# Kernel optimization log

Hardware: AMD Instinct MI355X
Metric: run time of the kernel (lower is better)

Reference implementation:

```python
import jax, jax.numpy as jnp
import numpy as np

B, K, W, H = 32, 64, 100, 150
ALPHA = 0.2        # leaky-relu slope
THRES = 2e-4       # causal threshold


def setup_inputs() -> dict:
    ks = jax.random.split(jax.random.key(0), 20)
    s = 0.1
    inp = {
        "x": jax.random.normal(ks[0], (B, K, W), jnp.float32),
        "y": jax.random.normal(ks[1], (B, K, 1), jnp.float32),
        "z_noise": jax.random.normal(ks[2], (B, H), jnp.float32),
        "lin_w": jax.random.normal(ks[3], (W, W), jnp.float32) * s,
        "lin_b": jax.random.normal(ks[4], (W,), jnp.float32) * s,
        "a": jax.random.normal(ks[5], (2, 1), jnp.float32),
        "bias": jax.random.normal(ks[6], (K, K * W), jnp.float32) * 0.01,
        "gl_wih": jax.random.normal(ks[7], (3 * H, W), jnp.float32) * s,
        "gl_whh": jax.random.normal(ks[8], (3 * H, H), jnp.float32) * s,
        "gl_bih": jax.random.normal(ks[9], (3 * H,), jnp.float32) * s,
        "gl_bhh": jax.random.normal(ks[10], (3 * H,), jnp.float32) * s,
        "mu_w": jax.random.normal(ks[11], (H, H), jnp.float32) * s,
        "mu_b": jax.random.normal(ks[12], (H,), jnp.float32) * s,
        "std_w": jax.random.normal(ks[13], (H, H), jnp.float32) * s,
        "std_b": jax.random.normal(ks[14], (H,), jnp.float32) * s,
        "net_wih": jax.random.normal(ks[15], (K, 3 * H, W), jnp.float32) * s,
        "net_whh": jax.random.normal(ks[16], (K, 3 * H, H), jnp.float32) * s,
        "net_bih": jax.random.normal(ks[17], (K, 3 * H), jnp.float32) * s,
        "net_bhh": jax.random.normal(ks[18], (K, 3 * H), jnp.float32) * s,
    }
    return inp


def _gru_last(wih, whh, bih, bhh, xs, h0):
    # xs: [B, S, in], h0: [B, H] -> final hidden [B, H]. PyTorch gate order r,z,n.
    gx = jnp.einsum('bsi,gi->sbg', xs, wih) + bih  # [S, B, 3H]
    h_dim = h0.shape[-1]

    def step(h, g):
        gh = h @ whh.T + bhh
        r = jax.nn.sigmoid(g[:, :h_dim] + gh[:, :h_dim])
        z = jax.nn.sigmoid(g[:, h_dim:2 * h_dim] + gh[:, h_dim:2 * h_dim])
        n = jnp.tanh(g[:, 2 * h_dim:] + r * gh[:, 2 * h_dim:])
        return (1.0 - z) * n + z * h, None

    h_last, _ = jax.lax.scan(step, h0, gx)
    return h_last


def reference(x, y, z_noise, lin_w, lin_b, a, bias, gl_wih, gl_whh, gl_bih, gl_bhh,
              mu_w, mu_b, std_w, std_b, net_wih, net_whh, net_bih, net_bhh):
    xw = x[:, :, -W:]
    Wx = xw @ lin_w.T + lin_b                       # [B, K, W]
    v = Wx.reshape(Wx.shape[0], K * W)              # [B, K*W]
    # e = a_input @ a, where a_input[...,0]=y broadcast, a_input[...,1]=v tiled per node
    e = a[0, 0] * y + a[1, 0] * v[:, None, :] + bias  # [B, K, K*W]
    e = jax.nn.leaky_relu(e, ALPHA)
    attention = jax.nn.softmax(e, axis=2)           # dropout p=0 -> identity
    A = attention >= THRES                           # [B, K, K*W] mask
    Ax = jnp.where(A, v[:, None, :], 0.0)
    cause_x = Wx + Ax.sum(axis=2, keepdims=True)    # [B, K, W]
    # left GRU over the node dimension (seq len = K)
    h0 = jnp.zeros((cause_x.shape[0], H), cause_x.dtype)
    h_t = _gru_last(gl_wih, gl_whh, gl_bih, gl_bhh, cause_x, h0)  # [B, H]
    mu = h_t @ mu_w.T + mu_b
    log_var = h_t @ std_w.T + std_b
    sigma = jnp.exp(0.5 * log_var)
    z = mu + sigma * z_noise                        # [B, H]
    # K independent GRUs, same input Wx and same init state z -> vmap over weights
    causes = jax.vmap(lambda wi, wh, bi, bh: _gru_last(wi, wh, bi, bh, Wx, z))(
        net_wih, net_whh, net_bih, net_bhh)         # [K, B, H]
    return causes.transpose(1, 0, 2)                # [B, K, H]
```

## Files before the change

kernel.cpp:

```cpp
#include <hip/hip_runtime.h>

#define Bc 32
#define Kc 64
#define Wc 100
#define Hc 150
#define H3c 450
#define KWc 6400
#define ALPHAc 0.2f
#define THRESc 0.0002f

typedef unsigned int u32;
typedef unsigned short u16;
typedef __attribute__((ext_vector_type(8))) short short8;
typedef __attribute__((ext_vector_type(4))) float floatx4;

#define OFF_WX      0u
#define OFF_CS      204800u
#define OFF_GX      206848u
#define OFF_HT      1128448u
#define OFF_Z       1133248u

__device__ __forceinline__ float us2f(u16 u){ u32 x=((u32)u)<<16; return __uint_as_float(x); }
__device__ __forceinline__ u16 f2us(float f){
  u32 x = __float_as_uint(f);
  u32 r = (x + 0x7fffu + ((x>>16)&1u)) >> 16;
  return (u16)r;
}

__device__ __forceinline__ void lds_barrier(){
  __builtin_amdgcn_sched_barrier(0);
  asm volatile("s_waitcnt lgkmcnt(0)" ::: "memory");
  __builtin_amdgcn_s_barrier();
  __builtin_amdgcn_sched_barrier(0);
}

__global__ void wx_kernel(const float* __restrict__ x, const float* __restrict__ lin_w,
                          const float* __restrict__ lin_b, float* __restrict__ ws){
  int o = blockIdx.x*256 + threadIdx.x;
  if (o >= Bc*KWc) return;
  int i = o % Wc;
  int bk = o / Wc;
  const float4* xr = (const float4*)(x + bk*Wc);
  const float4* wr = (const float4*)(lin_w + i*Wc);
  float acc = lin_b[i];
  #pragma unroll
  for (int j=0;j<25;j++){
    float4 xv = xr[j], wv = wr[j];
    acc += xv.x*wv.x + xv.y*wv.y + xv.z*wv.z + xv.w*wv.w;
  }
  ws[OFF_WX + o] = acc;
}

__global__ void attn_kernel(const float* __restrict__ y, const float* __restrict__ a,
                            const float* __restrict__ bias, float* __restrict__ ws){
  __shared__ __align__(16) float e_l[KWc];
  __shared__ float red[4];
  int row = blockIdx.x;
  int b = row >> 6, k = row & 63;
  int tid = threadIdx.x;
  float a0 = a[0], a1 = a[1];
  float yv = y[row];
  const float4* v4  = (const float4*)(ws + OFF_WX + (size_t)b*KWc);
  const float4* br4 = (const float4*)(bias + (size_t)k*KWc);
  float4* e4 = (float4*)e_l;
  float ay = a0*yv;
  float m = -3.4e38f;
  for (int j=tid; j<KWc/4; j+=256){
    float4 vv = v4[j], bb = br4[j];
    float4 e;
    e.x = ay + a1*vv.x + bb.x; e.x = (e.x>=0.f)?e.x:ALPHAc*e.x;
    e.y = ay + a1*vv.y + bb.y; e.y = (e.y>=0.f)?e.y:ALPHAc*e.y;
    e.z = ay + a1*vv.z + bb.z; e.z = (e.z>=0.f)?e.z:ALPHAc*e.z;
    e.w = ay + a1*vv.w + bb.w; e.w = (e.w>=0.f)?e.w:ALPHAc*e.w;
    e4[j] = e;
    m = fmaxf(m, fmaxf(fmaxf(e.x,e.y), fmaxf(e.z,e.w)));
  }
  for (int o=32;o;o>>=1) m = fmaxf(m, __shfl_down(m, o));
  if ((tid&63)==0) red[tid>>6] = m;
  __syncthreads();
  m = fmaxf(fmaxf(red[0],red[1]), fmaxf(red[2],red[3]));
  __syncthreads();
  float ssum = 0.f;
  for (int j=tid; j<KWc/4; j+=256){
    float4 e = e4[j];
    ssum += __expf(e.x-m) + __expf(e.y-m) + __expf(e.z-m) + __expf(e.w-m);
  }
  for (int o=32;o;o>>=1) ssum += __shfl_down(ssum, o);
  if ((tid&63)==0) red[tid>>6] = ssum;
  __syncthreads();
  float s = red[0]+red[1]+red[2]+red[3];
  float thr = m + logf(THRESc * s);
  float cs = 0.f;
  for (int j=tid; j<KWc/4; j+=256){
    float4 e = e4[j];
    float4 vv = v4[j];
    if (e.x >= thr) cs += vv.x;
    if (e.y >= thr) cs += vv.y;
    if (e.z >= thr) cs += vv.z;
    if (e.w >= thr) cs += vv.w;
  }
  for (int o=32;o;o>>=1) cs += __shfl_down(cs, o);
  if ((tid&63)==0) red[tid>>6] = cs;
  __syncthreads();
  if (tid==0) ws[OFF_CS + row] = red[0]+red[1]+red[2]+red[3];
}

__global__ void glproj_kernel(const float* __restrict__ gl_wih, const float* __restrict__ gl_bih,
                              float* __restrict__ ws){
  int o = blockIdx.x*256 + threadIdx.x;
  if (o >= Kc*Bc*H3c) return;
  int g = o % H3c;
  int t = o / H3c;
  int b = t & 31, s = t >> 5;
  float cs = ws[OFF_CS + b*Kc + s];
  const float4* xr = (const float4*)(ws + OFF_WX + b*KWc + s*Wc);
  const float4* wr = (const float4*)(gl_wih + g*Wc);
  float acc = gl_bih[g];
  #pragma unroll
  for (int j=0;j<25;j++){
    float4 wv = wr[j], xv = xr[j];
    acc += (xv.x+cs)*wv.x + (xv.y+cs)*wv.y + (xv.z+cs)*wv.z + (xv.w+cs)*wv.w;
  }
  ws[OFF_GX + o] = acc;
}

__global__ void __launch_bounds__(1024,1) glgru4_kernel(
    const float* __restrict__ gl_whh, const float* __restrict__ gl_bhh,
    float* __restrict__ ws){
  __shared__ __align__(16) u16 bF[10*16*40];
  __shared__ float g_l[480*10];
  int b0 = blockIdx.x*8;
  int tid = threadIdx.x;
  int w = tid >> 6, lane = tid & 63, quad = lane >> 4, n16 = lane & 15;

  short8 whhA[2][5];
  #pragma unroll
  for (int ti=0; ti<2; ti++){
    int tile = w*2 + ti;
    int sec = tile/10;
    int sr = (tile - sec*10)*16 + n16;
    bool rowok = (tile < 30) && (sr < Hc);
    int grow = (sec<3 ? sec : 2)*Hc + sr;
    const float* wr = gl_whh + (size_t)grow*Hc;
    #pragma unroll
    for (int c=0;c<5;c++){
      union { short8 v; u16 u[8]; } t8;
      #pragma unroll
      for (int j2=0;j2<4;j2++){
        int kk2 = c*32 + quad*8 + j2*2;
        float2 wv = (rowok && (kk2+1) < Hc) ? *(const float2*)(wr + kk2) : make_float2(0.f,0.f);
        t8.u[j2*2]   = f2us(wv.x);
        t8.u[j2*2+1] = f2us(wv.y);
      }
      whhA[ti][c] = t8.v;
    }
  }
  for (int i=tid; i<10*16*40/2; i+=1024) ((u32*)bF)[i] = 0u;

  float hst[2] = {0.f,0.f};
  float bh_r[2], bh_z[2], bh_n[2];
  int tT[2], tBL[2];
  #pragma unroll
  for (int q=0;q<2;q++){
    int task = tid + q*1024;
    if (task < 1200){
      int bl = task/150, t = task - bl*150;
      tT[q] = t; tBL[q] = bl;
      bh_r[q] = gl_bhh[t];
      bh_z[q] = gl_bhh[Hc+t];
      bh_n[q] = gl_bhh[2*Hc+t];
    } else { tT[q] = 0; tBL[q] = -1; }
  }

  for (int s=0;s<Kc;s++){
    lds_barrier();
    float gxr[2], gxz[2], gxn[2];
    const float* gxb = ws + OFF_GX + (size_t)(s*Bc)*H3c;
    #pragma unroll
    for (int q=0;q<2;q++){
      if (tBL[q] >= 0){
        const float* gp = gxb + (size_t)(b0+tBL[q])*H3c;
        int t = tT[q];
        gxr[q] = gp[t]; gxz[q] = gp[Hc+t]; gxn[q] = gp[2*Hc+t];
      }
    }
    const u16* bBase = bF + (size_t)n16*40 + (size_t)quad*8;
    short8 bh[10];
    #pragma unroll
    for (int c=0;c<10;c++) bh[c] = *(const short8*)(bBase + (size_t)c*640);
    floatx4 acc[2] = {{0.f,0.f,0.f,0.f},{0.f,0.f,0.f,0.f}};
    #pragma unroll
    for (int c=0;c<10;c++){
      int ca = (c<5)? c : (c-5);
      #pragma unroll
      for (int ti=0;ti<2;ti++)
        acc[ti] = __builtin_amdgcn_mfma_f32_16x16x32_bf16(whhA[ti][ca], bh[c], acc[ti], 0,0,0);
    }
    if (n16 < 8){
      #pragma unroll
      for (int ti=0;ti<2;ti++){
        int tile = w*2 + ti;
        if (tile < 30){
          int row0 = tile*16 + quad*4;
          float* gp = g_l + row0*10 + n16;
          #pragma unroll
          for (int r=0;r<4;r++) gp[r*10] = acc[ti][r];
        }
      }
    }
    lds_barrier();
    #pragma unroll
    for (int q=0;q<2;q++){
      if (tBL[q] >= 0){
        int t = tT[q], bl = tBL[q];
        float a_r = gxr[q] + g_l[t*10+bl] + bh_r[q];
        float a_z = gxz[q] + g_l[(160+t)*10+bl] + bh_z[q];
        float r  = 1.f/(1.f+__expf(-a_r));
        float zz = 1.f/(1.f+__expf(-a_z));
        float nx = gxn[q] + r*(g_l[(320+t)*10+bl] + bh_n[q]);
        nx = fminf(fmaxf(nx,-15.f),15.f);
        float e2 = __expf(2.f*nx);
        float n = (e2-1.f)/(e2+1.f);
        float h = (1.f-zz)*n + zz*hst[q];
        hst[q] = h;
        u16 hi = f2us(h); float hif = us2f(hi); u16 lo = f2us(h - hif);
        bF[(t>>5)*640 + bl*40 + (t&31)] = hi;
        bF[(5+(t>>5))*640 + bl*40 + (t&31)] = lo;
      }
    }
  }
  #pragma unroll
  for (int q=0;q<2;q++){
    if (tBL[q] >= 0)
      ws[OFF_HT + (size_t)(b0+tBL[q])*Hc + tT[q]] = hst[q];
  }
}

__global__ void z_kernel(const float* __restrict__ z_noise, const float* __restrict__ mu_w,
                         const float* __restrict__ mu_b, const float* __restrict__ std_w,
                         const float* __restrict__ std_b, float* __restrict__ ws){
  int o = blockIdx.x*256 + threadIdx.x;
  if (o >= Bc*Hc) return;
  int t = o % Hc, b = o / Hc;
  const float* h = ws + OFF_HT + b*Hc;
  const float2* mwr = (const float2*)(mu_w + t*Hc);
  const float2* swr = (const float2*)(std_w + t*Hc);
  float mu = mu_b[t], lv = std_b[t];
  for (int j=0;j<Hc/2;j++){
    float2 mw = mwr[j], sw = swr[j];
    float h0 = h[2*j], h1 = h[2*j+1];
    mu += h0*mw.x + h1*mw.y;
    lv += h0*sw.x + h1*sw.y;
  }
  float sg = expf(0.5f*lv);
  ws[OFF_Z + o] = mu + sg*z_noise[o];
}

__global__ void __launch_bounds__(1024,1) causes3_kernel(
    const float* __restrict__ net_wih, const float* __restrict__ net_whh,
    const float* __restrict__ net_bih, const float* __restrict__ net_bhh,
    const float* __restrict__ ws, float* __restrict__ out){
  __shared__ __align__(16) u16 bF[14*16*40];
  __shared__ float g_rz[320*10];
  __shared__ float g_nh[160*10];
  __shared__ float g_np[160*10];
  int kk = blockIdx.x & 63, bg = blockIdx.x >> 6, b0 = bg*8;
  int tid = threadIdx.x;
  int w = tid >> 6, lane = tid & 63, quad = lane >> 4, n16 = lane & 15;
  const float* whhk = net_whh + (size_t)kk*H3c*Hc;
  const float* wihk = net_wih + (size_t)kk*H3c*Wc;
  const float* bihk = net_bih + kk*H3c;
  const float* bhhk = net_bhh + kk*H3c;

  short8 whhA[2][5], wihA[2][4];
  #pragma unroll
  for (int ti=0; ti<2; ti++){
    int tile = w*2 + ti;
    int sec = tile/10;
    int sr = (tile - sec*10)*16 + n16;
    bool rowok = (tile < 30) && (sr < Hc);
    int grow = (sec<3 ? sec : 2)*Hc + sr;
    #pragma unroll
    for (int c=0;c<5;c++){
      union { short8 v; u16 u[8]; } t8;
      #pragma unroll
      for (int j=0;j<8;j++){
        int k = c*32 + quad*8 + j;
        float v = (rowok && k < Hc) ? whhk[(size_t)grow*Hc + k] : 0.f;
        t8.u[j] = f2us(v);
      }
      whhA[ti][c] = t8.v;
    }
    #pragma unroll
    for (int c=0;c<4;c++){
      union { short8 v; u16 u[8]; } t8;
      #pragma unroll
      for (int j=0;j<8;j++){
        int k = c*32 + quad*8 + j;
        float v = (rowok && k < Wc) ? wihk[(size_t)grow*Wc + k] : 0.f;
        t8.u[j] = f2us(v);
      }
      wihA[ti][c] = t8.v;
    }
  }

  for (int i=tid; i<14*16*40/2; i+=1024) ((u32*)bF)[i] = 0u;

  float hst[2] = {0.f,0.f};
  float brz_r[2], brz_z[2], bnh_[2], bnp_[2];
  #pragma unroll
  for (int q=0;q<2;q++){
    int task = tid + q*1024;
    if (task < 1200){
      int t = task >> 3, bb = task & 7;
      float h = ws[OFF_Z + (b0+bb)*Hc + t];
      hst[q] = h;
      brz_r[q] = bhhk[t]      + bihk[t];
      brz_z[q] = bhhk[Hc+t]   + bihk[Hc+t];
      bnh_[q]  = bhhk[2*Hc+t];
      bnp_[q]  = bihk[2*Hc+t];
      u16 hi = f2us(h); float hif = us2f(hi); u16 lo = f2us(h - hif);
      bF[(t>>5)*640 + bb*40 + (t&31)] = hi;
      bF[(5+(t>>5))*640 + bb*40 + (t&31)] = lo;
    } else { tT_dummy: ; }
  }
  if (tid < 800){
    int bb = tid/100, i = tid - bb*100;
    float xv = ws[OFF_WX + (b0+bb)*KWc + i];
    bF[(10+(i>>5))*640 + bb*40 + (i&31)] = f2us(xv);
  }

  bool xok = (tid < 800);
  int bb0 = xok ? tid/100 : 0;
  int i0  = tid - bb0*100;

  const bool isN = (w >= 10);
  for (int s=0;s<Kc;s++){
    float xp0 = 0.f;
    if (xok && s < Kc-1)
      xp0 = ws[OFF_WX + (size_t)(b0+bb0)*KWc + (s+1)*Wc + i0];
    lds_barrier();
    const u16* bBase = bF + (size_t)n16*40 + (size_t)quad*8;
    short8 bx[4];
    #pragma unroll
    for (int c=0;c<4;c++) bx[c] = *(const short8*)(bBase + (size_t)(10+c)*640);
    floatx4 acc[2] = {{0.f,0.f,0.f,0.f},{0.f,0.f,0.f,0.f}};
    #pragma unroll
    for (int ca=0;ca<4;ca++){
      #pragma unroll
      for (int ti=0;ti<2;ti++)
        acc[ti] = __builtin_amdgcn_mfma_f32_16x16x32_bf16(wihA[ti][ca], bx[ca], acc[ti], 0,0,0);
    }
    __builtin_amdgcn_sched_barrier(0);
    short8 bh0[5];
    #pragma unroll
    for (int c=0;c<5;c++) bh0[c] = *(const short8*)(bBase + (size_t)c*640);
    if (isN){
      if (n16 < 8){
        #pragma unroll
        for (int ti=0;ti<2;ti++){
          int tile = w*2 + ti;
          if (tile < 30){
            int srb = (tile - 20)*16 + quad*4;
            float* gq = g_np + srb*10 + n16;
            #pragma unroll
            for (int r=0;r<4;r++) gq[r*10] = acc[ti][r];
          }
        }
      }
      #pragma unroll
      for (int ti=0;ti<2;ti++) acc[ti] = (floatx4){0.f,0.f,0.f,0.f};
    }
    #pragma unroll
    for (int c=0;c<5;c++){
      #pragma unroll
      for (int ti=0;ti<2;ti++)
        acc[ti] = __builtin_amdgcn_mfma_f32_16x16x32_bf16(whhA[ti][c], bh0[c], acc[ti], 0,0,0);
    }
    __builtin_amdgcn_sched_barrier(0);
    short8 bh1[5];
    #pragma unroll
    for (int c=0;c<5;c++) bh1[c] = *(const short8*)(bBase + (size_t)(5+c)*640);
    #pragma unroll
    for (int c=0;c<5;c++){
      #pragma unroll
      for (int ti=0;ti<2;ti++)
        acc[ti] = __builtin_amdgcn_mfma_f32_16x16x32_bf16(whhA[ti][c], bh1[c], acc[ti], 0,0,0);
    }
    if (n16 < 8){
      #pragma unroll
      for (int ti=0;ti<2;ti++){
        int tile = w*2 + ti;
        if (tile < 30){
          int sec = tile/10;
          int srb = (tile - sec*10)*16 + quad*4;
          if (sec < 2){
            float* gp = g_rz + (sec*160 + srb)*10 + n16;
            #pragma unroll
            for (int r=0;r<4;r++) gp[r*10] = acc[ti][r];
          } else {
            float* gh = g_nh + srb*10 + n16;
            #pragma unroll
            for (int r=0;r<4;r++) gh[r*10] = acc[ti][r];
          }
        }
      }
    }
    lds_barrier();
    #pragma unroll
    for (int q=0;q<2;q++){
      int task = tid + q*1024;
      if (task < 1200){
        int t = task >> 3, bb = task & 7;
        float a_r = g_rz[t*10+bb] + brz_r[q];
        float a_z = g_rz[(160+t)*10+bb] + brz_z[q];
        float r  = 1.f/(1.f+__expf(-a_r));
        float zz = 1.f/(1.f+__expf(-a_z));
        float nx = (g_np[t*10+bb] + bnp_[q]) + r*(g_nh[t*10+bb] + bnh_[q]);
        nx = fminf(fmaxf(nx,-15.f),15.f);
        float e2 = __expf(2.f*nx);
        float n = (e2-1.f)/(e2+1.f);
        float h = (1.f-zz)*n + zz*hst[q];
        hst[q] = h;
        u16 hi = f2us(h); float hif = us2f(hi); u16 lo = f2us(h - hif);
        bF[(t>>5)*640 + bb*40 + (t&31)] = hi;
        bF[(5+(t>>5))*640 + bb*40 + (t&31)] = lo;
      }
    }
    if (xok && s < Kc-1)
      bF[(10+(i0>>5))*640 + bb0*40 + (i0&31)] = f2us(xp0);
  }
  #pragma unroll
  for (int q=0;q<2;q++){
    int task = tid + q*1024;
    if (task < 1200){
      int t = task >> 3, bb = task & 7;
      out[((size_t)(b0+bb)*Kc + kk)*Hc + t] = hst[q];
    }
  }
}

extern "C" void kernel_launch(void* const* d_in, const int* in_sizes, int n_in,
                              void* d_out, int out_size, void* d_ws, size_t ws_size,
                              hipStream_t stream){
  const float* x        = (const float*)d_in[0];
  const float* y        = (const float*)d_in[1];
  const float* z_noise  = (const float*)d_in[2];
  const float* lin_w    = (const float*)d_in[3];
  const float* lin_b    = (const float*)d_in[4];
  const float* a        = (const float*)d_in[5];
  const float* bias     = (const float*)d_in[6];
  const float* gl_wih   = (const float*)d_in[7];
  const float* gl_whh   = (const float*)d_in[8];
  const float* gl_bih   = (const float*)d_in[9];
  const float* gl_bhh   = (const float*)d_in[10];
  const float* mu_w     = (const float*)d_in[11];
  const float* mu_b     = (const float*)d_in[12];
  const float* std_w    = (const float*)d_in[13];
  const float* std_b    = (const float*)d_in[14];
  const float* net_wih  = (const float*)d_in[15];
  const float* net_whh  = (const float*)d_in[16];
  const float* net_bih  = (const float*)d_in[17];
  const float* net_bhh  = (const float*)d_in[18];
  float* ws = (float*)d_ws;
  float* out = (float*)d_out;

  wx_kernel<<<(Bc*KWc+255)/256, 256, 0, stream>>>(x, lin_w, lin_b, ws);
  attn_kernel<<<Bc*Kc, 256, 0, stream>>>(y, a, bias, ws);
  glproj_kernel<<<(Kc*Bc*H3c+255)/256, 256, 0, stream>>>(gl_wih, gl_bih, ws);
  glgru4_kernel<<<4, 1024, 0, stream>>>(gl_whh, gl_bhh, ws);
  z_kernel<<<(Bc*Hc+255)/256, 256, 0, stream>>>(z_noise, mu_w, mu_b, std_w, std_b, ws);
  causes3_kernel<<<Kc*4, 1024, 0, stream>>>(net_wih, net_whh, net_bih, net_bhh, ws, out);
}
```

Before: 487.8 us.

## Give each wave all three gates per hidden range; double-buffer state to drop barrier

```diff
diff --git a/kernel.cpp b/kernel.cpp
--- a/kernel.cpp
+++ b/kernel.cpp
@@ -11,6 +11,7 @@
 
 typedef unsigned int u32;
 typedef unsigned short u16;
+typedef unsigned long long u64;
 typedef __attribute__((ext_vector_type(8))) short short8;
 typedef __attribute__((ext_vector_type(4))) float floatx4;
 
@@ -124,115 +125,110 @@
   ws[OFF_GX + o] = acc;
 }
 
-__global__ void __launch_bounds__(1024,1) glgru4_kernel(
+__global__ void __launch_bounds__(640,1) glgru4_kernel(
     const float* __restrict__ gl_whh, const float* __restrict__ gl_bhh,
     float* __restrict__ ws){
-  __shared__ __align__(16) u16 bF[10*16*40];
-  __shared__ float g_l[480*10];
+  __shared__ __align__(16) u16 bF[20*16*40];
   int b0 = blockIdx.x*8;
   int tid = threadIdx.x;
   int w = tid >> 6, lane = tid & 63, quad = lane >> 4, n16 = lane & 15;
-
-  short8 whhA[2][5];
-  #pragma unroll
-  for (int ti=0; ti<2; ti++){
-    int tile = w*2 + ti;
-    int sec = tile/10;
-    int sr = (tile - sec*10)*16 + n16;
-    bool rowok = (tile < 30) && (sr < Hc);
-    int grow = (sec<3 ? sec : 2)*Hc + sr;
-    const float* wr = gl_whh + (size_t)grow*Hc;
+  int range = w;
+  int t0 = range*16 + quad*4;
+
+  short8 whhA[3][5];
+  #pragma unroll
+  for (int sec=0; sec<3; sec++){
+    int sr = range*16 + n16;
+    bool rowok = (sr < Hc);
+    const float* wr = gl_whh + (size_t)(sec*Hc + sr)*Hc;
     #pragma unroll
     for (int c=0;c<5;c++){
       union { short8 v; u16 u[8]; } t8;
       #pragma unroll
-      for (int j2=0;j2<4;j2++){
-        int kk2 = c*32 + quad*8 + j2*2;
-        float2 wv = (rowok && (kk2+1) < Hc) ? *(const float2*)(wr + kk2) : make_float2(0.f,0.f);
-        t8.u[j2*2]   = f2us(wv.x);
-        t8.u[j2*2+1] = f2us(wv.y);
-      }
-      whhA[ti][c] = t8.v;
-    }
-  }
-  for (int i=tid; i<10*16*40/2; i+=1024) ((u32*)bF)[i] = 0u;
-
-  float hst[2] = {0.f,0.f};
-  float bh_r[2], bh_z[2], bh_n[2];
-  int tT[2], tBL[2];
-  #pragma unroll
-  for (int q=0;q<2;q++){
-    int task = tid + q*1024;
-    if (task < 1200){
-      int bl = task/150, t = task - bl*150;
-      tT[q] = t; tBL[q] = bl;
-      bh_r[q] = gl_bhh[t];
-      bh_z[q] = gl_bhh[Hc+t];
-      bh_n[q] = gl_bhh[2*Hc+t];
-    } else { tT[q] = 0; tBL[q] = -1; }
+      for (int j=0;j<8;j++){
+        int k = c*32 + quad*8 + j;
+        float v = (rowok && k < Hc) ? wr[k] : 0.f;
+        t8.u[j] = f2us(v);
+      }
+      whhA[sec][c] = t8.v;
+    }
+  }
+  for (int i=tid; i<20*640/2; i+=640) ((u32*)bF)[i] = 0u;
+
+  float bh_r[4], bh_z[4], bh_n[4], hprev[4];
+  #pragma unroll
+  for (int r=0;r<4;r++){
+    int t = t0 + r;
+    bool ok = (t < Hc);
+    bh_r[r] = ok ? gl_bhh[t]      : 0.f;
+    bh_z[r] = ok ? gl_bhh[Hc+t]   : 0.f;
+    bh_n[r] = ok ? gl_bhh[2*Hc+t] : 0.f;
+    hprev[r] = 0.f;
   }
 
   for (int s=0;s<Kc;s++){
+    int rb = s & 1, wb = rb ^ 1;
+    float gxr[4], gxz[4], gxn[4];
+    if (n16 < 8){
+      const float* gp = ws + OFF_GX + (size_t)(s*Bc + b0 + n16)*H3c;
+      #pragma unroll
+      for (int r=0;r<4;r++){
+        int t = t0 + r;
+        bool ok = (t < Hc);
+        gxr[r] = ok ? gp[t]      : 0.f;
+        gxz[r] = ok ? gp[Hc+t]   : 0.f;
+        gxn[r] = ok ? gp[2*Hc+t] : 0.f;
+      }
+    }
     lds_barrier();
-    float gxr[2], gxz[2], gxn[2];
-    const float* gxb = ws + OFF_GX + (size_t)(s*Bc)*H3c;
-    #pragma unroll
-    for (int q=0;q<2;q++){
-      if (tBL[q] >= 0){
-        const float* gp = gxb + (size_t)(b0+tBL[q])*H3c;
-        int t = tT[q];
-        gxr[q] = gp[t]; gxz[q] = gp[Hc+t]; gxn[q] = gp[2*Hc+t];
-      }
-    }
-    const u16* bBase = bF + (size_t)n16*40 + (size_t)quad*8;
-    short8 bh[10];
-    #pragma unroll
-    for (int c=0;c<10;c++) bh[c] = *(const short8*)(bBase + (size_t)c*640);
-    floatx4 acc[2] = {{0.f,0.f,0.f,0.f},{0.f,0.f,0.f,0.f}};
-    #pragma unroll
-    for (int c=0;c<10;c++){
-      int ca = (c<5)? c : (c-5);
-      #pragma unroll
-      for (int ti=0;ti<2;ti++)
-        acc[ti] = __builtin_amdgcn_mfma_f32_16x16x32_bf16(whhA[ti][ca], bh[c], acc[ti], 0,0,0);
+    const u16* hBase = bF + (size_t)rb*6400 + (size_t)(n16&7)*40 + (size_t)(n16>>3)*3200 + (size_t)quad*8;
+    short8 bh[5];
+    #pragma unroll
+    for (int c=0;c<5;c++) bh[c] = *(const short8*)(hBase + (size_t)c*640);
+    floatx4 accR={0.f,0.f,0.f,0.f}, accZ={0.f,0.f,0.f,0.f}, accNH={0.f,0.f,0.f,0.f};
+    #pragma unroll
+    for (int c=0;c<5;c++){
+      accR  = __builtin_amdgcn_mfma_f32_16x16x32_bf16(whhA[0][c], bh[c], accR, 0,0,0);
+      accZ  = __builtin_amdgcn_mfma_f32_16x16x32_bf16(whhA[1][c], bh[c], accZ, 0,0,0);
+      accNH = __builtin_amdgcn_mfma_f32_16x16x32_bf16(whhA[2][c], bh[c], accNH, 0,0,0);
+    }
+    #pragma unroll
+    for (int r=0;r<4;r++){
+      accR[r]  += __shfl_xor(accR[r], 8);
+      accZ[r]  += __shfl_xor(accZ[r], 8);
+      accNH[r] += __shfl_xor(accNH[r], 8);
     }
     if (n16 < 8){
-      #pragma unroll
-      for (int ti=0;ti<2;ti++){
-        int tile = w*2 + ti;
-        if (tile < 30){
-          int row0 = tile*16 + quad*4;
-          float* gp = g_l + row0*10 + n16;
-          #pragma unroll
-          for (int r=0;r<4;r++) gp[r*10] = acc[ti][r];
-        }
-      }
-    }
-    lds_barrier();
-    #pragma unroll
-    for (int q=0;q<2;q++){
-      if (tBL[q] >= 0){
-        int t = tT[q], bl = tBL[q];
-        float a_r = gxr[q] + g_l[t*10+bl] + bh_r[q];
-        float a_z = gxz[q] + g_l[(160+t)*10+bl] + bh_z[q];
-        float r  = 1.f/(1.f+__expf(-a_r));
+      float hout[4];
+      #pragma unroll
+      for (int r=0;r<4;r++){
+        float a_r = gxr[r] + accR[r] + bh_r[r];
+        float a_z = gxz[r] + accZ[r] + bh_z[r];
+        float rr = 1.f/(1.f+__expf(-a_r));
         float zz = 1.f/(1.f+__expf(-a_z));
-        float nx = gxn[q] + r*(g_l[(320+t)*10+bl] + bh_n[q]);
+        float nx = gxn[r] + rr*(accNH[r] + bh_n[r]);
         nx = fminf(fmaxf(nx,-15.f),15.f);
         float e2 = __expf(2.f*nx);
         float n = (e2-1.f)/(e2+1.f);
-        float h = (1.f-zz)*n + zz*hst[q];
-        hst[q] = h;
-        u16 hi = f2us(h); float hif = us2f(hi); u16 lo = f2us(h - hif);
-        bF[(t>>5)*640 + bl*40 + (t&31)] = hi;
-        bF[(5+(t>>5))*640 + bl*40 + (t&31)] = lo;
-      }
-    }
-  }
-  #pragma unroll
-  for (int q=0;q<2;q++){
-    if (tBL[q] >= 0)
-      ws[OFF_HT + (size_t)(b0+tBL[q])*Hc + tT[q]] = hst[q];
+        float h = (1.f-zz)*n + zz*hprev[r];
+        hprev[r] = h; hout[r] = h;
+      }
+      u16 h0=f2us(hout[0]), h1=f2us(hout[1]), h2=f2us(hout[2]), h3=f2us(hout[3]);
+      u16 l0=f2us(hout[0]-us2f(h0)), l1=f2us(hout[1]-us2f(h1));
+      u16 l2=f2us(hout[2]-us2f(h2)), l3=f2us(hout[3]-us2f(h3));
+      u64 hiP = (u64)h0 | ((u64)h1<<16) | ((u64)h2<<32) | ((u64)h3<<48);
+      u64 loP = (u64)l0 | ((u64)l1<<16) | ((u64)l2<<32) | ((u64)l3<<48);
+      u32 wbase = (u32)wb*6400u + (u32)(t0>>5)*640u + (u32)n16*40u + (u32)(t0&31);
+      *(u64*)(bF + wbase)        = hiP;
+      *(u64*)(bF + wbase + 3200) = loP;
+    }
+  }
+  if (n16 < 8){
+    #pragma unroll
+    for (int r=0;r<4;r++){
+      int t = t0 + r;
+      if (t < Hc) ws[OFF_HT + (size_t)(b0+n16)*Hc + t] = hprev[r];
+    }
   }
 }
 
@@ -256,40 +252,39 @@
   ws[OFF_Z + o] = mu + sg*z_noise[o];
 }
 
-__global__ void __launch_bounds__(1024,1) causes3_kernel(
+__global__ void __launch_bounds__(640,1) causes3_kernel(
     const float* __restrict__ net_wih, const float* __restrict__ net_whh,
     const float* __restrict__ net_bih, const float* __restrict__ net_bhh,
     const float* __restrict__ ws, float* __restrict__ out){
-  __shared__ __align__(16) u16 bF[14*16*40];
-  __shared__ float g_rz[320*10];
-  __shared__ float g_nh[160*10];
-  __shared__ float g_np[160*10];
+  __shared__ __align__(16) u16 bF[28*16*40];
+  const u32 XB = 20*640u;
   int kk = blockIdx.x & 63, bg = blockIdx.x >> 6, b0 = bg*8;
   int tid = threadIdx.x;
   int w = tid >> 6, lane = tid & 63, quad = lane >> 4, n16 = lane & 15;
+  int range = w;
+  int t0 = range*16 + quad*4;
   const float* whhk = net_whh + (size_t)kk*H3c*Hc;
   const float* wihk = net_wih + (size_t)kk*H3c*Wc;
   const float* bihk = net_bih + kk*H3c;
   const float* bhhk = net_bhh + kk*H3c;
 
-  short8 whhA[2][5], wihA[2][4];
-  #pragma unroll
-  for (int ti=0; ti<2; ti++){
-    int tile = w*2 + ti;
-    int sec = tile/10;
-    int sr = (tile - sec*10)*16 + n16;
-    bool rowok = (tile < 30) && (sr < Hc);
-    int grow = (sec<3 ? sec : 2)*Hc + sr;
+  short8 whhA[3][5], wihA[3][4];
+  #pragma unroll
+  for (int sec=0; sec<3; sec++){
+    int sr = range*16 + n16;
+    bool rowok = (sr < Hc);
+    const float* wr  = whhk + (size_t)(sec*Hc + sr)*Hc;
+    const float* wr2 = wihk + (size_t)(sec*Hc + sr)*Wc;
     #pragma unroll
     for (int c=0;c<5;c++){
       union { short8 v; u16 u[8]; } t8;
       #pragma unroll
       for (int j=0;j<8;j++){
         int k = c*32 + quad*8 + j;
-        float v = (rowok && k < Hc) ? whhk[(size_t)grow*Hc + k] : 0.f;
+        float v = (rowok && k < Hc) ? wr[k] : 0.f;
         t8.u[j] = f2us(v);
       }
-      whhA[ti][c] = t8.v;
+      whhA[sec][c] = t8.v;
     }
     #pragma unroll
     for (int c=0;c<4;c++){
@@ -297,145 +292,116 @@
       #pragma unroll
       for (int j=0;j<8;j++){
         int k = c*32 + quad*8 + j;
-        float v = (rowok && k < Wc) ? wihk[(size_t)grow*Wc + k] : 0.f;
+        float v = (rowok && k < Wc) ? wr2[k] : 0.f;
         t8.u[j] = f2us(v);
       }
-      wihA[ti][c] = t8.v;
-    }
-  }
-
-  for (int i=tid; i<14*16*40/2; i+=1024) ((u32*)bF)[i] = 0u;
-
-  float hst[2] = {0.f,0.f};
-  float brz_r[2], brz_z[2], bnh_[2], bnp_[2];
-  #pragma unroll
-  for (int q=0;q<2;q++){
-    int task = tid + q*1024;
-    if (task < 1200){
-      int t = task >> 3, bb = task & 7;
-      float h = ws[OFF_Z + (b0+bb)*Hc + t];
-      hst[q] = h;
-      brz_r[q] = bhhk[t]      + bihk[t];
-      brz_z[q] = bhhk[Hc+t]   + bihk[Hc+t];
-      bnh_[q]  = bhhk[2*Hc+t];
-      bnp_[q]  = bihk[2*Hc+t];
-      u16 hi = f2us(h); float hif = us2f(hi); u16 lo = f2us(h - hif);
-      bF[(t>>5)*640 + bb*40 + (t&31)] = hi;
-      bF[(5+(t>>5))*640 + bb*40 + (t&31)] = lo;
-    } else { tT_dummy: ; }
-  }
-  if (tid < 800){
-    int bb = tid/100, i = tid - bb*100;
-    float xv = ws[OFF_WX + (b0+bb)*KWc + i];
-    bF[(10+(i>>5))*640 + bb*40 + (i&31)] = f2us(xv);
-  }
-
-  bool xok = (tid < 800);
-  int bb0 = xok ? tid/100 : 0;
-  int i0  = tid - bb0*100;
-
-  const bool isN = (w >= 10);
+      wihA[sec][c] = t8.v;
+    }
+  }
+
+  for (int i=tid; i<28*640/2; i+=640) ((u32*)bF)[i] = 0u;
+
+  float brz_r[4], brz_z[4], bnp_[4], bnh_[4], hprev[4];
+  #pragma unroll
+  for (int r=0;r<4;r++){
+    int t = t0 + r;
+    bool ok = (t < Hc);
+    brz_r[r] = ok ? (bhhk[t]      + bihk[t])      : 0.f;
+    brz_z[r] = ok ? (bhhk[Hc+t]   + bihk[Hc+t])   : 0.f;
+    bnh_[r]  = ok ? bhhk[2*Hc+t] : 0.f;
+    bnp_[r]  = ok ? bihk[2*Hc+t] : 0.f;
+    hprev[r] = (ok && n16 < 8) ? ws[OFF_Z + (size_t)(b0+n16)*Hc + t] : 0.f;
+  }
+  __syncthreads();
+
+  for (int item=tid; item<1200; item+=640){
+    int t = item >> 3, bb = item & 7;
+    float h = ws[OFF_Z + (size_t)(b0+bb)*Hc + t];
+    u16 hi = f2us(h); u16 lo = f2us(h - us2f(hi));
+    bF[(t>>5)*640 + bb*40 + (t&31)] = hi;
+    bF[3200 + (t>>5)*640 + bb*40 + (t&31)] = lo;
+  }
+  for (int item=tid; item<800; item+=640){
+    int bb = item/100, i = item - bb*100;
+    bF[XB + (i>>5)*640 + bb*40 + (i&31)] = f2us(ws[OFF_WX + (size_t)(b0+bb)*KWc + i]);
+  }
+
+  int bb0 = tid/100, i0 = tid - bb0*100;
+  int it1 = tid + 640;
+  int bb1 = it1/100, i1 = it1 - bb1*100;
+  bool v1ok = (it1 < 800);
+
   for (int s=0;s<Kc;s++){
-    float xp0 = 0.f;
-    if (xok && s < Kc-1)
+    int rb = s & 1, wb = rb ^ 1;
+    float xp0=0.f, xp1=0.f;
+    if (s < Kc-1){
       xp0 = ws[OFF_WX + (size_t)(b0+bb0)*KWc + (s+1)*Wc + i0];
+      if (v1ok) xp1 = ws[OFF_WX + (size_t)(b0+bb1)*KWc + (s+1)*Wc + i1];
+    }
     lds_barrier();
-    const u16* bBase = bF + (size_t)n16*40 + (size_t)quad*8;
+    const u16* xBase = bF + XB + (size_t)rb*2560 + (size_t)n16*40 + (size_t)quad*8;
+    const u16* hBase = bF + (size_t)rb*6400 + (size_t)(n16&7)*40 + (size_t)(n16>>3)*3200 + (size_t)quad*8;
     short8 bx[4];
     #pragma unroll
-    for (int c=0;c<4;c++) bx[c] = *(const short8*)(bBase + (size_t)(10+c)*640);
-    floatx4 acc[2] = {{0.f,0.f,0.f,0.f},{0.f,0.f,0.f,0.f}};
-    #pragma unroll
-    for (int ca=0;ca<4;ca++){
-      #pragma unroll
-      for (int ti=0;ti<2;ti++)
-        acc[ti] = __builtin_amdgcn_mfma_f32_16x16x32_bf16(wihA[ti][ca], bx[ca], acc[ti], 0,0,0);
+    for (int c=0;c<4;c++) bx[c] = *(const short8*)(xBase + (size_t)c*640);
+    floatx4 accR={0.f,0.f,0.f,0.f}, accZ={0.f,0.f,0.f,0.f};
+    floatx4 accNP={0.f,0.f,0.f,0.f}, accNH={0.f,0.f,0.f,0.f};
+    #pragma unroll
+    for (int c=0;c<4;c++){
+      accR  = __builtin_amdgcn_mfma_f32_16x16x32_bf16(wihA[0][c], bx[c], accR, 0,0,0);
+      accZ  = __builtin_amdgcn_mfma_f32_16x16x32_bf16(wihA[1][c], bx[c], accZ, 0,0,0);
+      accNP = __builtin_amdgcn_mfma_f32_16x16x32_bf16(wihA[2][c], bx[c], accNP, 0,0,0);
     }
     __builtin_amdgcn_sched_barrier(0);
-    short8 bh0[5];
-    #pragma unroll
-    for (int c=0;c<5;c++) bh0[c] = *(const short8*)(bBase + (size_t)c*640);
-    if (isN){
-      if (n16 < 8){
-        #pragma unroll
-        for (int ti=0;ti<2;ti++){
-          int tile = w*2 + ti;
-          if (tile < 30){
-            int srb = (tile - 20)*16 + quad*4;
-            float* gq = g_np + srb*10 + n16;
-            #pragma unroll
-            for (int r=0;r<4;r++) gq[r*10] = acc[ti][r];
-          }
-        }
-      }
-      #pragma unroll
-      for (int ti=0;ti<2;ti++) acc[ti] = (floatx4){0.f,0.f,0.f,0.f};
-    }
+    short8 bh[5];
+    #pragma unroll
+    for (int c=0;c<5;c++) bh[c] = *(const short8*)(hBase + (size_t)c*640);
     #pragma unroll
     for (int c=0;c<5;c++){
-      #pragma unroll
-      for (int ti=0;ti<2;ti++)
-        acc[ti] = __builtin_amdgcn_mfma_f32_16x16x32_bf16(whhA[ti][c], bh0[c], acc[ti], 0,0,0);
-    }
-    __builtin_amdgcn_sched_barrier(0);
-    short8 bh1[5];
-    #pragma unroll
-    for (int c=0;c<5;c++) bh1[c] = *(const short8*)(bBase + (size_t)(5+c)*640);
-    #pragma unroll
-    for (int c=0;c<5;c++){
-      #pragma unroll
-      for (int ti=0;ti<2;ti++)
-        acc[ti] = __builtin_amdgcn_mfma_f32_16x16x32_bf16(whhA[ti][c], bh1[c], acc[ti], 0,0,0);
+      accR  = __builtin_amdgcn_mfma_f32_16x16x32_bf16(whhA[0][c], bh[c], accR, 0,0,0);
+      accZ  = __builtin_amdgcn_mfma_f32_16x16x32_bf16(whhA[1][c], bh[c], accZ, 0,0,0);
+      accNH = __builtin_amdgcn_mfma_f32_16x16x32_bf16(whhA[2][c], bh[c], accNH, 0,0,0);
+    }
+    #pragma unroll
+    for (int r=0;r<4;r++){
+      accR[r]  += __shfl_xor(accR[r], 8);
+      accZ[r]  += __shfl_xor(accZ[r], 8);
+      accNH[r] += __shfl_xor(accNH[r], 8);
     }
     if (n16 < 8){
-      #pragma unroll
-      for (int ti=0;ti<2;ti++){
-        int tile = w*2 + ti;
-        if (tile < 30){
-          int sec = tile/10;
-          int srb = (tile - sec*10)*16 + quad*4;
-          if (sec < 2){
-            float* gp = g_rz + (sec*160 + srb)*10 + n16;
-            #pragma unroll
-            for (int r=0;r<4;r++) gp[r*10] = acc[ti][r];
-          } else {
-            float* gh = g_nh + srb*10 + n16;
-            #pragma unroll
-            for (int r=0;r<4;r++) gh[r*10] = acc[ti][r];
-          }
-        }
-      }
-    }
-    lds_barrier();
-    #pragma unroll
-    for (int q=0;q<2;q++){
-      int task = tid + q*1024;
-      if (task < 1200){
-        int t = task >> 3, bb = task & 7;
-        float a_r = g_rz[t*10+bb] + brz_r[q];
-        float a_z = g_rz[(160+t)*10+bb] + brz_z[q];
-        float r  = 1.f/(1.f+__expf(-a_r));
+      float hout[4];
+      #pragma unroll
+      for (int r=0;r<4;r++){
+        float a_r = accR[r] + brz_r[r];
+        float a_z = accZ[r] + brz_z[r];
+        float rr = 1.f/(1.f+__expf(-a_r));
         float zz = 1.f/(1.f+__expf(-a_z));
-        float nx = (g_np[t*10+bb] + bnp_[q]) + r*(g_nh[t*10+bb] + bnh_[q]);
+        float nx = (accNP[r] + bnp_[r]) + rr*(accNH[r] + bnh_[r]);
         nx = fminf(fmaxf(nx,-15.f),15.f);
         float e2 = __expf(2.f*nx);
         float n = (e2-1.f)/(e2+1.f);
-        float h = (1.f-zz)*n + zz*hst[q];
-        hst[q] = h;
-        u16 hi = f2us(h); float hif = us2f(hi); u16 lo = f2us(h - hif);
-        bF[(t>>5)*640 + bb*40 + (t&31)] = hi;
-        bF[(5+(t>>5))*640 + bb*40 + (t&31)] = lo;
-      }
-    }
-    if (xok && s < Kc-1)
-      bF[(10+(i0>>5))*640 + bb0*40 + (i0&31)] = f2us(xp0);
-  }
-  #pragma unroll
-  for (int q=0;q<2;q++){
-    int task = tid + q*1024;
-    if (task < 1200){
-      int t = task >> 3, bb = task & 7;
-      out[((size_t)(b0+bb)*Kc + kk)*Hc + t] = hst[q];
+        float h = (1.f-zz)*n + zz*hprev[r];
+        hprev[r] = h; hout[r] = h;
+      }
+      u16 h0=f2us(hout[0]), h1=f2us(hout[1]), h2=f2us(hout[2]), h3=f2us(hout[3]);
+      u16 l0=f2us(hout[0]-us2f(h0)), l1=f2us(hout[1]-us2f(h1));
+      u16 l2=f2us(hout[2]-us2f(h2)), l3=f2us(hout[3]-us2f(h3));
+      u64 hiP = (u64)h0 | ((u64)h1<<16) | ((u64)h2<<32) | ((u64)h3<<48);
+      u64 loP = (u64)l0 | ((u64)l1<<16) | ((u64)l2<<32) | ((u64)l3<<48);
+      u32 wbase = (u32)wb*6400u + (u32)(t0>>5)*640u + (u32)n16*40u + (u32)(t0&31);
+      *(u64*)(bF + wbase)        = hiP;
+      *(u64*)(bF + wbase + 3200) = loP;
+      if (s == Kc-1){
+        #pragma unroll
+        for (int r=0;r<4;r++){
+          int t = t0 + r;
+          if (t < Hc) out[((size_t)(b0+n16)*Kc + kk)*Hc + t] = hout[r];
+        }
+      }
+    }
+    if (s < Kc-1){
+      bF[XB + wb*2560 + (i0>>5)*640 + bb0*40 + (i0&31)] = f2us(xp0);
+      if (v1ok) bF[XB + wb*2560 + (i1>>5)*640 + bb1*40 + (i1&31)] = f2us(xp1);
     }
   }
 }
@@ -468,7 +434,7 @@
   wx_kernel<<<(Bc*KWc+255)/256, 256, 0, stream>>>(x, lin_w, lin_b, ws);
   attn_kernel<<<Bc*Kc, 256, 0, stream>>>(y, a, bias, ws);
   glproj_kernel<<<(Kc*Bc*H3c+255)/256, 256, 0, stream>>>(gl_wih, gl_bih, ws);
-  glgru4_kernel<<<4, 1024, 0, stream>>>(gl_whh, gl_bhh, ws);
+  glgru4_kernel<<<4, 640, 0, stream>>>(gl_whh, gl_bhh, ws);
   z_kernel<<<(Bc*Hc+255)/256, 256, 0, stream>>>(z_noise, mu_w, mu_b, std_w, std_b, ws);
-  causes3_kernel<<<Kc*4, 1024, 0, stream>>>(net_wih, net_whh, net_bih, net_bhh, ws, out);
-}
+  causes3_kernel<<<Kc*4, 640, 0, stream>>>(net_wih, net_whh, net_bih, net_bhh, ws, out);
+}
```

Measured after the change: 554.8 us. +13.7%, slower.
